# Optimization experiments

Measured on AMD Instinct MI355X. Metric: run time of the kernel, lower is better.

The kernel has to match this reference:

```python
import jax, jax.numpy as jnp
import numpy as np

BATCH = 131072
N = 64          # total bits
PARTS = 16      # len(partition) == dpp_size
M = 4           # bits per part
D = PARTS
EPS = 1e-8


def _colnorm(a):
    return a / jnp.linalg.norm(a, axis=0, keepdims=True)


def setup_inputs() -> dict:
    key = jax.random.key(0)
    k0, k1, k2, k3, k4 = jax.random.split(key, 5)
    x = jax.random.randint(k0, (BATCH, N), 0, 2, dtype=jnp.int32)
    W = jax.random.normal(k1, (PARTS, (1 << M) - 1), dtype=jnp.float32)
    A = _colnorm(jax.random.normal(k2, (D, D), dtype=jnp.float32))
    B = _colnorm(jax.random.normal(k3, (D, D), dtype=jnp.float32))
    C = _colnorm(jax.random.normal(k4, (D, D), dtype=jnp.float32))
    return {"x": x, "W": W, "A": A, "B": B, "C": C}


def reference(x, W, A, B, C):
    batch = x.shape[0]
    # --- Simple PCs (vectorized over the 16 parts): bit-pack each 4-bit part ---
    bits = x.reshape(batch, PARTS, M)                       # contiguous partition
    pow2 = (1 << jnp.arange(M)).astype(jnp.int32)           # [M]
    idx = jnp.sum(bits * pow2, axis=-1)                     # [B, P] in [0, 2^M)
    w = jax.nn.softmax(W, axis=-1)                          # [P, 2^M - 1]
    w = jnp.concatenate([jnp.zeros((PARTS, 1), w.dtype), w], axis=-1)  # [P, 2^M]
    p = w[jnp.arange(PARTS)[None, :], idx]                  # [B, P]

    # --- L matrix: sym PD part + skew part ---
    I = jnp.eye(D, dtype=A.dtype)
    L0 = A.T @ A + (B @ C.T - C @ B.T) + EPS * I            # [D, D]

    # column-scale by p, then force diagonal to 1 where p == 0
    Lp = L0[None, :, :] * p[:, None, :]                     # [B, D, D]
    eye_b = jnp.eye(D, dtype=bool)
    mask = eye_b[None, :, :] & (p == 0.0)[:, :, None]
    Lp = jnp.where(mask, jnp.asarray(1.0, Lp.dtype), Lp)

    sign, logabs = jnp.linalg.slogdet(Lp)                   # [B]
    y = logabs + jnp.log(jax.lax.stop_gradient(sign))       # nan if det < 0 (matches torch.logdet)
    s0, la0 = jnp.linalg.slogdet(L0 + I)
    alpha = la0 + jnp.log(jax.lax.stop_gradient(s0))
    return y - alpha
```

## Files before the change

### kernel.cpp

```cpp
#include <hip/hip_runtime.h>
#include <math.h>

#define BATCH 131072
#define EPS 1e-8f


__global__ void prep_kernel(const float* W, const float* A, const float* Bm,
                            const float* Cm, float* ws) {
    int t = threadIdx.x;
    int i = t >> 4, j = t & 15;
    float s = 0.f;
    #pragma unroll
    for (int k = 0; k < 16; ++k) {
        s += A[k * 16 + i] * A[k * 16 + j];
        s += Bm[i * 16 + k] * Cm[j * 16 + k]
           - Cm[i * 16 + k] * Bm[j * 16 + k];
    }
    if (i == j) s += EPS;
    ws[t] = s;

    if (t < 16) {
        float row[15];
        float mx = -1e30f;
        #pragma unroll
        for (int q = 0; q < 15; ++q) { row[q] = W[t * 15 + q]; mx = fmaxf(mx, row[q]); }
        float se = 0.f;
        #pragma unroll
        for (int q = 0; q < 15; ++q) se += expf(row[q] - mx);
        float lse = mx + logf(se);
        ws[256 + t * 16 + 0] = 0.f;
        #pragma unroll
        for (int q = 0; q < 15; ++q) ws[256 + t * 16 + 1 + q] = row[q] - lse;
    }
}

__global__ __launch_bounds__(64, 1) void table_kernel(const float* ws, float* T,
                                                      float* alphaOut) {
    __shared__ float sL0[256];
    int lt = threadIdx.x;
    #pragma unroll
    for (int q = 0; q < 4; ++q) sL0[lt * 4 + q] = ws[lt * 4 + q];
    __syncthreads();

    unsigned tid = blockIdx.x * 64u + (unsigned)lt;
    if (tid > 65536u) return;
    bool isAlpha = (tid == 65536u);
    unsigned m = isAlpha ? 0xFFFFu : tid;

    float a[16][16];
    #pragma unroll
    for (int i = 0; i < 16; ++i) {
        bool ai = (m >> i) & 1u;
        #pragma unroll
        for (int j = 0; j < 16; ++j) {
            bool aj = (m >> j) & 1u;
            float v = (ai && aj) ? sL0[i * 16 + j] : ((i == j) ? 1.f : 0.f);
            if (isAlpha && i == j) v += 1.f;
            a[i][j] = v;
        }
    }

    float logdet = 0.f;
    #pragma unroll
    for (int k = 0; k < 16; ++k) {
        float piv = a[k][k];
        logdet += __logf(fabsf(piv));
        float inv = 1.0f / piv;
        #pragma unroll
        for (int i2 = k + 1; i2 < 16; ++i2) {
            float f = a[i2][k] * inv;
            #pragma unroll
            for (int j2 = k + 1; j2 < 16; ++j2)
                a[i2][j2] = fmaf(-f, a[k][j2], a[i2][j2]);
        }
    }

    if (isAlpha) *alphaOut = logdet;
    else         T[tid]    = logdet;
}

__global__ __launch_bounds__(256) void main_kernel(const int4* __restrict__ x,
                                                   const float* __restrict__ ws,
                                                   float* __restrict__ out) {
    __shared__ float slw[256];
    int lt = threadIdx.x;
    slw[lt] = ws[256 + lt];
    __syncthreads();

    int b = blockIdx.x * 256 + lt;
    const int4* xb = x + (size_t)b * 16;

    float lw = 0.f;
    unsigned mask = 0;
    #pragma unroll
    for (int j = 0; j < 16; ++j) {
        int4 v = xb[j];
        int idx = v.x + 2 * v.y + 4 * v.z + 8 * v.w;
        lw += slw[j * 16 + idx];
        mask |= (idx != 0 ? 1u : 0u) << j;
    }
    float alpha = ws[512];
    out[b] = lw + ws[1024 + mask] - alpha;
}

extern "C" void kernel_launch(void* const* d_in, const int* in_sizes, int n_in,
                              void* d_out, int out_size, void* d_ws, size_t ws_size,
                              hipStream_t stream) {
    const float* W = (const float*)d_in[1];
    const float* A = (const float*)d_in[2];
    const float* B = (const float*)d_in[3];
    const float* C = (const float*)d_in[4];
    const int4*  x = (const int4*)d_in[0];
    float* ws  = (float*)d_ws;
    float* out = (float*)d_out;

    prep_kernel<<<1, 256, 0, stream>>>(W, A, B, C, ws);
    table_kernel<<<1025, 64, 0, stream>>>(ws, ws + 1024, ws + 512);
    main_kernel<<<BATCH / 256, 256, 0, stream>>>(x, ws, out);
}
```

Baseline: 95.99 us.

## Split 65536-entry logdet table via Schur complement over high/low byte masks

Rather than running a full 16x16 LU for every one of the 65536 masks, the new code eliminates the 8 always-present rows once per high-byte mask (256 cases) and stores the 8x8 Schur complement plus the partial log-determinant. A second kernel then runs only an 8x8 LU per low-byte mask, with alpha folded into the table entries. The prep work is also merged into the first stage. This cuts table-building arithmetic and register pressure, at the cost of an extra global round trip for the intermediate Schur blocks and a changed workspace layout.

```diff
diff --git a/kernel.cpp b/kernel.cpp
--- a/kernel.cpp
+++ b/kernel.cpp
@@ -5,78 +5,144 @@
 #define EPS 1e-8f
 
 
-__global__ void prep_kernel(const float* W, const float* A, const float* Bm,
-                            const float* Cm, float* ws) {
-    int t = threadIdx.x;
-    int i = t >> 4, j = t & 15;
-    float s = 0.f;
+__global__ __launch_bounds__(64, 1) void stageA_kernel(const float* __restrict__ W,
+                                                       const float* __restrict__ A,
+                                                       const float* __restrict__ Bm,
+                                                       const float* __restrict__ Cm,
+                                                       float* __restrict__ ws) {
+    __shared__ float sL0[256];
+    int lt = threadIdx.x;
     #pragma unroll
-    for (int k = 0; k < 16; ++k) {
-        s += A[k * 16 + i] * A[k * 16 + j];
-        s += Bm[i * 16 + k] * Cm[j * 16 + k]
-           - Cm[i * 16 + k] * Bm[j * 16 + k];
+    for (int q = 0; q < 4; ++q) {
+        int e = lt * 4 + q;
+        int i = e >> 4, j = e & 15;
+        float s = 0.f;
+        #pragma unroll
+        for (int k = 0; k < 16; ++k) {
+            s += A[k * 16 + i] * A[k * 16 + j];
+            s += Bm[i * 16 + k] * Cm[j * 16 + k]
+               - Cm[i * 16 + k] * Bm[j * 16 + k];
+        }
+        if (i == j) s += EPS;
+        sL0[e] = s;
     }
-    if (i == j) s += EPS;
-    ws[t] = s;
+    __syncthreads();
 
-    if (t < 16) {
+    unsigned tg = blockIdx.x * 64u + (unsigned)lt;
+
+    if (tg >= 288u && tg < 304u) {
+        int r = (int)tg - 288;
         float row[15];
         float mx = -1e30f;
         #pragma unroll
-        for (int q = 0; q < 15; ++q) { row[q] = W[t * 15 + q]; mx = fmaxf(mx, row[q]); }
+        for (int q = 0; q < 15; ++q) { row[q] = W[r * 15 + q]; mx = fmaxf(mx, row[q]); }
         float se = 0.f;
         #pragma unroll
         for (int q = 0; q < 15; ++q) se += expf(row[q] - mx);
         float lse = mx + logf(se);
-        ws[256 + t * 16 + 0] = 0.f;
+        ws[r * 16 + 0] = 0.f;
         #pragma unroll
-        for (int q = 0; q < 15; ++q) ws[256 + t * 16 + 1 + q] = row[q] - lse;
+        for (int q = 0; q < 15; ++q) ws[r * 16 + 1 + q] = row[q] - lse;
+    }
+
+    if (tg > 256u) return;
+    bool isAlpha = (tg == 256u);
+    unsigned h = isAlpha ? 0xFFu : tg;
+
+    float a[16][16];
+    #pragma unroll
+    for (int r = 0; r < 16; ++r) {
+        int i = (r < 8) ? (8 + r) : (r - 8);
+        bool pi = (i < 8) ? true : (((h >> (i - 8)) & 1u) != 0u);
+        #pragma unroll
+        for (int c = 0; c < 16; ++c) {
+            int j = (c < 8) ? (8 + c) : (c - 8);
+            bool pj = (j < 8) ? true : (((h >> (j - 8)) & 1u) != 0u);
+            float v = (pi && pj) ? sL0[i * 16 + j] : ((r == c) ? 1.f : 0.f);
+            if (isAlpha && r == c) v += 1.f;
+            a[r][c] = v;
+        }
+    }
+
+    float plog = 0.f;
+    #pragma unroll
+    for (int k = 0; k < 8; ++k) {
+        float piv = a[k][k];
+        plog += __logf(fabsf(piv));
+        float inv = 1.0f / piv;
+        #pragma unroll
+        for (int r2 = k + 1; r2 < 16; ++r2) {
+            float f = a[r2][k] * inv;
+            #pragma unroll
+            for (int c2 = k + 1; c2 < 16; ++c2)
+                a[r2][c2] = fmaf(-f, a[k][c2], a[r2][c2]);
+        }
+    }
+
+    if (!isAlpha) {
+        #pragma unroll
+        for (int i = 0; i < 8; ++i)
+            #pragma unroll
+            for (int j = 0; j < 8; ++j)
+                ws[512 + h * 64 + i * 8 + j] = a[8 + i][8 + j];
+        ws[17408 + h] = plog;
+    } else {
+        #pragma unroll
+        for (int k = 8; k < 16; ++k) {
+            float piv = a[k][k];
+            plog += __logf(fabsf(piv));
+            float inv = 1.0f / piv;
+            #pragma unroll
+            for (int r2 = k + 1; r2 < 16; ++r2) {
+                float f = a[r2][k] * inv;
+                #pragma unroll
+                for (int c2 = k + 1; c2 < 16; ++c2)
+                    a[r2][c2] = fmaf(-f, a[k][c2], a[r2][c2]);
+            }
+        }
+        ws[256] = plog;
     }
 }
 
-__global__ __launch_bounds__(64, 1) void table_kernel(const float* ws, float* T,
-                                                      float* alphaOut) {
-    __shared__ float sL0[256];
+__global__ __launch_bounds__(256) void stageB_kernel(const float* __restrict__ ws,
+                                                     float* __restrict__ T) {
+    __shared__ float s8[64];
+    __shared__ float sp[2];
     int lt = threadIdx.x;
-    #pragma unroll
-    for (int q = 0; q < 4; ++q) sL0[lt * 4 + q] = ws[lt * 4 + q];
+    int b  = blockIdx.x;
+    if (lt < 64)  s8[lt] = ws[512 + b * 64 + lt];
+    if (lt == 64) sp[0] = ws[17408 + b];
+    if (lt == 65) sp[1] = ws[256];
     __syncthreads();
 
-    unsigned tid = blockIdx.x * 64u + (unsigned)lt;
-    if (tid > 65536u) return;
-    bool isAlpha = (tid == 65536u);
-    unsigned m = isAlpha ? 0xFFFFu : tid;
-
-    float a[16][16];
+    unsigned lo = (unsigned)lt;
+    float a[8][8];
     #pragma unroll
-    for (int i = 0; i < 16; ++i) {
-        bool ai = (m >> i) & 1u;
+    for (int i = 0; i < 8; ++i) {
+        bool bi = ((lo >> i) & 1u) != 0u;
         #pragma unroll
-        for (int j = 0; j < 16; ++j) {
-            bool aj = (m >> j) & 1u;
-            float v = (ai && aj) ? sL0[i * 16 + j] : ((i == j) ? 1.f : 0.f);
-            if (isAlpha && i == j) v += 1.f;
-            a[i][j] = v;
+        for (int j = 0; j < 8; ++j) {
+            bool bj = ((lo >> j) & 1u) != 0u;
+            a[i][j] = (bi && bj) ? s8[i * 8 + j] : ((i == j) ? 1.f : 0.f);
         }
     }
 
-    float logdet = 0.f;
+    float ld = sp[0] - sp[1];
     #pragma unroll
-    for (int k = 0; k < 16; ++k) {
+    for (int k = 0; k < 8; ++k) {
         float piv = a[k][k];
-        logdet += __logf(fabsf(piv));
+        ld += __logf(fabsf(piv));
         float inv = 1.0f / piv;
         #pragma unroll
-        for (int i2 = k + 1; i2 < 16; ++i2) {
-            float f = a[i2][k] * inv;
+        for (int i = k + 1; i < 8; ++i) {
+            float f = a[i][k] * inv;
             #pragma unroll
-            for (int j2 = k + 1; j2 < 16; ++j2)
-                a[i2][j2] = fmaf(-f, a[k][j2], a[i2][j2]);
+            for (int j = k + 1; j < 8; ++j)
+                a[i][j] = fmaf(-f, a[k][j], a[i][j]);
         }
     }
 
-    if (isAlpha) *alphaOut = logdet;
-    else         T[tid]    = logdet;
+    T[b * 256 + lt] = ld;
 }
 
 __global__ __launch_bounds__(256) void main_kernel(const int4* __restrict__ x,
@@ -84,7 +150,7 @@
                                                    float* __restrict__ out) {
     __shared__ float slw[256];
     int lt = threadIdx.x;
-    slw[lt] = ws[256 + lt];
+    slw[lt] = ws[lt];
     __syncthreads();
 
     int b = blockIdx.x * 256 + lt;
@@ -99,8 +165,7 @@
         lw += slw[j * 16 + idx];
         mask |= (idx != 0 ? 1u : 0u) << j;
     }
-    float alpha = ws[512];
-    out[b] = lw + ws[1024 + mask] - alpha;
+    out[b] = lw + ws[32768 + mask];
 }
 
 extern "C" void kernel_launch(void* const* d_in, const int* in_sizes, int n_in,
@@ -114,7 +179,7 @@
     float* ws  = (float*)d_ws;
     float* out = (float*)d_out;
 
-    prep_kernel<<<1, 256, 0, stream>>>(W, A, B, C, ws);
-    table_kernel<<<1025, 64, 0, stream>>>(ws, ws + 1024, ws + 512);
+    stageA_kernel<<<5, 64, 0, stream>>>(W, A, B, C, ws);
+    stageB_kernel<<<256, 256, 0, stream>>>(ws, ws + 32768);
     main_kernel<<<BATCH / 256, 256, 0, stream>>>(x, ws, out);
 }
```

New measurement: 90.42 us. -5.8%, faster.
